# Optimization experiments

Hardware: AMD Instinct MI355X
Metric: run time of the kernel (lower is better)

The kernel has to match this reference:

```python
import jax, jax.numpy as jnp
import numpy as np

DIM = 256
BETA = 4
B, L, L1 = 16, 2048, 4096
EPS = 1e-6


def setup_inputs() -> dict:
    key = jax.random.key(0)
    ks = jax.random.split(key, 20)
    d, db = DIM, DIM // BETA
    s = lambda *sh: 0.02
    inp = {
        "features": jax.random.normal(ks[0], (B, L, d), jnp.float32),
        "quires_box": jax.random.uniform(ks[1], (B, L1, 2), jnp.float32),
        "quires_features": jax.random.normal(ks[2], (B, L1, d), jnp.float32),
        "pos_feature": jax.random.normal(ks[3], (B, L1, d), jnp.float32),
        # contrast1 params
        "c1_w1": jax.random.normal(ks[4], (db, d), jnp.float32) * 0.02,
        "c1_b1": jnp.zeros((db,), jnp.float32),
        "c1_w2": jax.random.normal(ks[5], (d, db), jnp.float32) * 0.02,
        "c1_b2": jnp.zeros((d,), jnp.float32),
        "c1_g": jnp.ones((d,), jnp.float32),
        "c1_be": jnp.zeros((d,), jnp.float32),
        # contrast2 params
        "c2_w1": jax.random.normal(ks[6], (db, d), jnp.float32) * 0.02,
        "c2_b1": jnp.zeros((db,), jnp.float32),
        "c2_w2": jax.random.normal(ks[7], (d, db), jnp.float32) * 0.02,
        "c2_b2": jnp.zeros((d,), jnp.float32),
        "c2_g": jnp.ones((d,), jnp.float32),
        "c2_be": jnp.zeros((d,), jnp.float32),
        # gate MLP (Prediction: Linear(2d->d)+ReLU+Linear(d->2), dropout=identity at eval)
        "g_w1": jax.random.normal(ks[8], (d, 2 * d), jnp.float32) * 0.02,
        "g_b1": jnp.zeros((d,), jnp.float32),
        "g_w2": jax.random.normal(ks[9], (2, d), jnp.float32) * 0.02,
        "g_b2": jnp.zeros((2,), jnp.float32),
    }
    return inp


def _contrast(v1, v2, w1, b1, w2, b2, g, be):
    # v1, v2: [B, N, C]. Pointwise conv1 -> ReLU -> conv2 -> LayerNorm -> sigmoid -> *v1
    v = v1 * v2
    h = jax.nn.relu(jnp.einsum('bnc,dc->bnd', v, w1) + b1)  # [B,N,C/beta]
    u = jnp.einsum('bnd,cd->bnc', h, w2) + b2               # [B,N,C]
    mu = jnp.mean(u, axis=-1, keepdims=True)
    var = jnp.mean(jnp.square(u - mu), axis=-1, keepdims=True)
    ln = (u - mu) * jax.lax.rsqrt(var + EPS) * g + be
    return jax.nn.sigmoid(ln) * v1


def reference(features, quires_box, quires_features, pos_feature,
              c1_w1, c1_b1, c1_w2, c1_b2, c1_g, c1_be,
              c2_w1, c2_b1, c2_w2, c2_b2, c2_g, c2_be,
              g_w1, g_b1, g_w2, g_b2):
    Lf = features.shape[1]
    cx, w = quires_box[..., 0], quires_box[..., 1]
    roi_start = jnp.round(jnp.clip((cx - w / 2) * Lf, 0, Lf - 1)).astype(jnp.int32)
    roi_end = jnp.round(jnp.clip((cx + w / 2) * Lf, 0, Lf - 1)).astype(jnp.int32)
    sf = jnp.take_along_axis(features, roi_start[..., None], axis=1)  # [B,L1,C]
    ef = jnp.take_along_axis(features, roi_end[..., None], axis=1)    # [B,L1,C]
    sf = _contrast(sf, pos_feature, c1_w1, c1_b1, c1_w2, c1_b2, c1_g, c1_be)
    ef = _contrast(ef, pos_feature, c2_w1, c2_b1, c2_w2, c2_b2, c2_g, c2_be)
    pooled = (sf + ef) * 0.5  # aligned_len=True -> mean over the 2 boundaries
    x = jnp.concatenate([pooled, quires_features], axis=-1)  # [B,L1,2C]
    h = jax.nn.relu(jnp.einsum('bnc,dc->bnd', x, g_w1) + g_b1)
    gate = jax.nn.softmax(jnp.einsum('bnd,od->bno', h, g_w2) + g_b2, axis=-1)
    out = pooled * gate[..., 0:1] + quires_features * gate[..., 1:2]
    return jnp.swapaxes(out, 0, 1)  # [L1, B, C]
```

## Files before the change

kernel.cpp:

```cpp
#include <hip/hip_runtime.h>
#include <hip/hip_bf16.h>
#include <math.h>

typedef __attribute__((ext_vector_type(8))) short bf16x8;
typedef __attribute__((ext_vector_type(4))) float f32x4;
typedef __attribute__((ext_vector_type(2))) __fp16 f16x2;
typedef __attribute__((ext_vector_type(4))) unsigned int u32x4;
typedef __attribute__((ext_vector_type(2))) unsigned int u32x2;

constexpr int NB = 16, NQ = 4096, LF = 2048, C = 256;

__device__ __forceinline__ unsigned short bfbits(float x) {
    return __builtin_bit_cast(unsigned short, __float2bfloat16(x));
}
__device__ __forceinline__ unsigned pk2(float a, float b) {
    return (unsigned)bfbits(a) | ((unsigned)bfbits(b) << 16);
}
__device__ __forceinline__ float bflo(unsigned d) { return __builtin_bit_cast(float, d << 16); }
__device__ __forceinline__ float bfhi(unsigned d) { return __builtin_bit_cast(float, d & 0xffff0000u); }
__device__ __forceinline__ unsigned pkh(float a, float b) {
    f16x2 h = __builtin_amdgcn_cvt_pkrtz(a, b);
    return __builtin_bit_cast(unsigned, h);
}
__device__ __forceinline__ float hlo(unsigned u) {
    f16x2 h = __builtin_bit_cast(f16x2, u); return (float)h[0];
}
__device__ __forceinline__ float hhi(unsigned u) {
    f16x2 h = __builtin_bit_cast(f16x2, u); return (float)h[1];
}

__global__ void prep_weights(const float* __restrict__ c1w1, const float* __restrict__ c2w1,
                             const float* __restrict__ c1w2, const float* __restrict__ c2w2,
                             const float* __restrict__ gw1, unsigned short* __restrict__ ws)
{
    int t = blockIdx.x * 256 + threadIdx.x;
    const float* src; int K, nks, dstoff, f;
    if (t < 2048)      { src = c1w1; K = 256; nks = 8;  dstoff = 0;      f = t; }
    else if (t < 4096) { src = c2w1; K = 256; nks = 8;  dstoff = 16384;  f = t - 2048; }
    else if (t < 6144) { src = c1w2; K = 64;  nks = 2;  dstoff = 32768;  f = t - 4096; }
    else if (t < 8192) { src = c2w2; K = 64;  nks = 2;  dstoff = 49152;  f = t - 6144; }
    else               { src = gw1;  K = 512; nks = 16; dstoff = 65536;  f = t - 8192; }
    int l = f & 63, s = f >> 6;
    int nt = s / nks, ks = s % nks;
    int n  = nt * 16 + (l & 15);
    int k0 = ks * 32 + (l >> 4) * 8;
    unsigned short* d = ws + dstoff + (size_t)f * 8;
    const float* sp = src + (size_t)n * K + k0;
    #pragma unroll
    for (int e = 0; e < 8; ++e) d[e] = bfbits(sp[e]);
}

__global__ __launch_bounds__(256, 4)
void semalign_v13(const float* __restrict__ feat,  const float* __restrict__ qbox,
                  const float* __restrict__ qfeat, const float* __restrict__ posf,
                  const float* __restrict__ c1b1,  const float* __restrict__ c1b2,
                  const float* __restrict__ c1g,   const float* __restrict__ c1be,
                  const float* __restrict__ c2b1,  const float* __restrict__ c2b2,
                  const float* __restrict__ c2g,   const float* __restrict__ c2be,
                  const float* __restrict__ gb1,   const float* __restrict__ gw2,
                  const float* __restrict__ gb2,
                  const unsigned short* __restrict__ wsb,
                  float* __restrict__ out)
{
    __shared__ __align__(16) unsigned short sP[4][16][256];

    const int tid = threadIdx.x, l = tid & 63, wid = tid >> 6;
    const int lr = l & 15, lg = l >> 4;
    const int rowb = blockIdx.x * 64 + wid * 16;
    const int q = rowb >> 4;
    const int b = lr;
    const int swz = (lr & 7) << 4;

    const float* prow = posf  + ((size_t)b * NQ + q) * C;
    const float* qrow = qfeat + ((size_t)b * NQ + q) * C;
    float cx = qbox[((size_t)b * NQ + q) * 2 + 0];
    float w  = qbox[((size_t)b * NQ + q) * 2 + 1];
    float fs = fminf(fmaxf((cx - 0.5f * w) * (float)LF, 0.f), (float)(LF - 1));
    float fe = fminf(fmaxf((cx + 0.5f * w) * (float)LF, 0.f), (float)(LF - 1));
    const float* srow = feat + ((size_t)b * LF + (int)rintf(fs)) * C;
    const float* erow = feat + ((size_t)b * LF + (int)rintf(fe)) * C;

    bf16x8 v1f[8], v2f[8];
    #pragma unroll
    for (int ks = 0; ks < 8; ++ks) {
        int k0 = ks * 32 + lg * 8;
        float4 s0 = *(const float4*)(srow + k0), s1 = *(const float4*)(srow + k0 + 4);
        float4 e0 = *(const float4*)(erow + k0), e1 = *(const float4*)(erow + k0 + 4);
        float4 p0 = *(const float4*)(prow + k0), p1 = *(const float4*)(prow + k0 + 4);
        u32x4 a, c;
        a[0] = pk2(s0.x * p0.x, s0.y * p0.y); a[1] = pk2(s0.z * p0.z, s0.w * p0.w);
        a[2] = pk2(s1.x * p1.x, s1.y * p1.y); a[3] = pk2(s1.z * p1.z, s1.w * p1.w);
        c[0] = pk2(e0.x * p0.x, e0.y * p0.y); c[1] = pk2(e0.z * p0.z, e0.w * p0.w);
        c[2] = pk2(e1.x * p1.x, e1.y * p1.y); c[3] = pk2(e1.z * p1.z, e1.w * p1.w);
        v1f[ks] = __builtin_bit_cast(bf16x8, a);
        v2f[ks] = __builtin_bit_cast(bf16x8, c);
    }

    char* pb = (char*)&sP[wid][0][0];
    {
        f32x4 a1[4] = {}, a2[4] = {};
        #pragma unroll
        for (int ks = 0; ks < 8; ++ks) {
            #pragma unroll
            for (int nt = 0; nt < 4; ++nt) {
                bf16x8 wA = *(const bf16x8*)(wsb + ((size_t)((nt * 8 + ks) * 64 + l)) * 8);
                bf16x8 wB = *(const bf16x8*)(wsb + 16384 + ((size_t)((nt * 8 + ks) * 64 + l)) * 8);
                a1[nt] = __builtin_amdgcn_mfma_f32_16x16x32_bf16(wA, v1f[ks], a1[nt], 0, 0, 0);
                a2[nt] = __builtin_amdgcn_mfma_f32_16x16x32_bf16(wB, v2f[ks], a2[nt], 0, 0, 0);
            }
        }
        #pragma unroll
        for (int nt = 0; nt < 4; ++nt) {
            float4 b1v = *(const float4*)(c1b1 + nt * 16 + lg * 4);
            float4 b2v = *(const float4*)(c2b1 + nt * 16 + lg * 4);
            u32x2 wv;
            wv[0] = pk2(fmaxf(a1[nt][0] + b1v.x, 0.f), fmaxf(a1[nt][1] + b1v.y, 0.f));
            wv[1] = pk2(fmaxf(a1[nt][2] + b1v.z, 0.f), fmaxf(a1[nt][3] + b1v.w, 0.f));
            *(u32x2*)(pb + lr * 128 + ((nt * 32 + lg * 8) ^ swz)) = wv;
            wv[0] = pk2(fmaxf(a2[nt][0] + b2v.x, 0.f), fmaxf(a2[nt][1] + b2v.y, 0.f));
            wv[1] = pk2(fmaxf(a2[nt][2] + b2v.z, 0.f), fmaxf(a2[nt][3] + b2v.w, 0.f));
            *(u32x2*)(pb + 2048 + lr * 128 + ((nt * 32 + lg * 8) ^ swz)) = wv;
        }
    }

    f16x2 Ph[16][2];
    #pragma unroll
    for (int j = 0; j < 2; ++j) {
        char* hb = pb + j * 2048;
        asm volatile("s_waitcnt lgkmcnt(0)" ::: "memory");
        bf16x8 hf0 = *(const bf16x8*)(hb + lr * 128 + ((0 + lg * 16) ^ swz));
        bf16x8 hf1 = *(const bf16x8*)(hb + lr * 128 + ((64 + lg * 16) ^ swz));
        const unsigned short* w2b = wsb + (j ? 49152 : 32768);
        const float* b2p = j ? c2b2 : c1b2;
        const float* gp  = j ? c2g  : c1g;
        const float* bep = j ? c2be : c1be;
        const float* xrow = j ? erow : srow;
        float S = 0.f, Q2 = 0.f;

        {
            f32x4 u8[8] = {};
            #pragma unroll
            for (int nt = 0; nt < 8; ++nt) {
                bf16x8 wA = *(const bf16x8*)(w2b + ((size_t)((nt * 2 + 0) * 64 + l)) * 8);
                bf16x8 wB = *(const bf16x8*)(w2b + ((size_t)((nt * 2 + 1) * 64 + l)) * 8);
                u8[nt] = __builtin_amdgcn_mfma_f32_16x16x32_bf16(wA, hf0, u8[nt], 0, 0, 0);
                u8[nt] = __builtin_amdgcn_mfma_f32_16x16x32_bf16(wB, hf1, u8[nt], 0, 0, 0);
            }
            #pragma unroll
            for (int nt = 0; nt < 8; ++nt) {
                float4 bv = *(const float4*)(b2p + nt * 16 + lg * 4);
                u8[nt][0] += bv.x; u8[nt][1] += bv.y; u8[nt][2] += bv.z; u8[nt][3] += bv.w;
                S  += u8[nt][0] + u8[nt][1] + u8[nt][2] + u8[nt][3];
                Q2 += u8[nt][0] * u8[nt][0] + u8[nt][1] * u8[nt][1]
                    + u8[nt][2] * u8[nt][2] + u8[nt][3] * u8[nt][3];
                u32x2 wv;
                wv[0] = pkh(u8[nt][0], u8[nt][1]);
                wv[1] = pkh(u8[nt][2], u8[nt][3]);
                *(u32x2*)(pb + 4096 + nt * 512 + l * 8) = wv;
            }
        }
        f32x4 u8b[8] = {};
        #pragma unroll
        for (int nt = 0; nt < 8; ++nt) {
            bf16x8 wA = *(const bf16x8*)(w2b + ((size_t)(((nt + 8) * 2 + 0) * 64 + l)) * 8);
            bf16x8 wB = *(const bf16x8*)(w2b + ((size_t)(((nt + 8) * 2 + 1) * 64 + l)) * 8);
            u8b[nt] = __builtin_amdgcn_mfma_f32_16x16x32_bf16(wA, hf0, u8b[nt], 0, 0, 0);
            u8b[nt] = __builtin_amdgcn_mfma_f32_16x16x32_bf16(wB, hf1, u8b[nt], 0, 0, 0);
        }
        #pragma unroll
        for (int nt = 0; nt < 8; ++nt) {
            float4 bv = *(const float4*)(b2p + (nt + 8) * 16 + lg * 4);
            u8b[nt][0] += bv.x; u8b[nt][1] += bv.y; u8b[nt][2] += bv.z; u8b[nt][3] += bv.w;
            S  += u8b[nt][0] + u8b[nt][1] + u8b[nt][2] + u8b[nt][3];
            Q2 += u8b[nt][0] * u8b[nt][0] + u8b[nt][1] * u8b[nt][1]
                + u8b[nt][2] * u8b[nt][2] + u8b[nt][3] * u8b[nt][3];
        }
        S  += __shfl_xor(S, 16);  S  += __shfl_xor(S, 32);
        Q2 += __shfl_xor(Q2, 16); Q2 += __shfl_xor(Q2, 32);
        float mu  = S * (1.f / 256.f);
        float rsg = rsqrtf(Q2 * (1.f / 256.f) - mu * mu + 1e-6f);

        u32x2 st[8];
        asm volatile("s_waitcnt lgkmcnt(0)" ::: "memory");
        #pragma unroll
        for (int nt = 0; nt < 8; ++nt)
            st[nt] = *(const u32x2*)(pb + 4096 + nt * 512 + l * 8);
        asm volatile("s_waitcnt lgkmcnt(0)" ::: "memory");

        #pragma unroll
        for (int nt = 0; nt < 16; ++nt) {
            float u4[4];
            if (nt < 8) {
                u4[0] = hlo(st[nt][0]); u4[1] = hhi(st[nt][0]);
                u4[2] = hlo(st[nt][1]); u4[3] = hhi(st[nt][1]);
            } else {
                u4[0] = u8b[nt - 8][0]; u4[1] = u8b[nt - 8][1];
                u4[2] = u8b[nt - 8][2]; u4[3] = u8b[nt - 8][3];
            }
            float4 gv  = *(const float4*)(gp  + nt * 16 + lg * 4);
            float4 bev = *(const float4*)(bep + nt * 16 + lg * 4);
            float4 xv  = *(const float4*)(xrow + nt * 16 + lg * 4);
            float g4[4] = { gv.x, gv.y, gv.z, gv.w };
            float e4[4] = { bev.x, bev.y, bev.z, bev.w };
            float x4[4] = { xv.x, xv.y, xv.z, xv.w };
            float tm[4];
            #pragma unroll
            for (int r = 0; r < 4; ++r) {
                float ln = (u4[r] - mu) * rsg * g4[r] + e4[r];
                float sg = 1.f / (1.f + __expf(-ln));
                tm[r] = 0.5f * sg * x4[r];
            }
            if (j == 0) {
                Ph[nt][0] = __builtin_amdgcn_cvt_pkrtz(tm[0], tm[1]);
                Ph[nt][1] = __builtin_amdgcn_cvt_pkrtz(tm[2], tm[3]);
            } else {
                float p0 = (float)Ph[nt][0][0] + tm[0];
                float p1 = (float)Ph[nt][0][1] + tm[1];
                float p2 = (float)Ph[nt][1][0] + tm[2];
                float p3 = (float)Ph[nt][1][1] + tm[3];
                u32x2 wv;
                wv[0] = pk2(p0, p1); wv[1] = pk2(p2, p3);
                *(u32x2*)(pb + lr * 512 + ((nt * 32 + lg * 8) ^ swz)) = wv;
            }
        }
    }

    bf16x8 xf[16];
    asm volatile("s_waitcnt lgkmcnt(0)" ::: "memory");
    #pragma unroll
    for (int ks = 0; ks < 8; ++ks)
        xf[ks] = *(const bf16x8*)(pb + lr * 512 + ((ks * 64 + lg * 16) ^ swz));
    #pragma unroll
    for (int ks = 0; ks < 8; ++ks) {
        int k0 = ks * 32 + lg * 8;
        float4 q0 = *(const float4*)(qrow + k0), q1 = *(const float4*)(qrow + k0 + 4);
        u32x4 a;
        a[0] = pk2(q0.x, q0.y); a[1] = pk2(q0.z, q0.w);
        a[2] = pk2(q1.x, q1.y); a[3] = pk2(q1.z, q1.w);
        xf[8 + ks] = __builtin_bit_cast(bf16x8, a);
    }

    float t0 = 0.f, t1 = 0.f;
    const unsigned short* gwb = wsb + 65536;
    for (int ntp = 0; ntp < 8; ++ntp) {
        f32x4 ga0 = {}, ga1 = {};
        int n0 = ntp * 2, n1 = ntp * 2 + 1;
        #pragma unroll
        for (int kk = 0; kk < 16; ++kk) {
            bf16x8 wA = *(const bf16x8*)(gwb + ((size_t)((n0 * 16 + kk) * 64 + l)) * 8);
            bf16x8 wB = *(const bf16x8*)(gwb + ((size_t)((n1 * 16 + kk) * 64 + l)) * 8);
            ga0 = __builtin_amdgcn_mfma_f32_16x16x32_bf16(wA, xf[kk], ga0, 0, 0, 0);
            ga1 = __builtin_amdgcn_mfma_f32_16x16x32_bf16(wB, xf[kk], ga1, 0, 0, 0);
        }
        #pragma unroll
        for (int t = 0; t < 2; ++t) {
            f32x4 ga = t ? ga1 : ga0;
            int nt = ntp * 2 + t;
            float4 gbv = *(const float4*)(gb1 + nt * 16 + lg * 4);
            float4 w0v = *(const float4*)(gw2 + nt * 16 + lg * 4);
            float4 w1v = *(const float4*)(gw2 + 256 + nt * 16 + lg * 4);
            float gb4[4] = { gbv.x, gbv.y, gbv.z, gbv.w };
            float w04[4] = { w0v.x, w0v.y, w0v.z, w0v.w };
            float w14[4] = { w1v.x, w1v.y, w1v.z, w1v.w };
            #pragma unroll
            for (int r = 0; r < 4; ++r) {
                float hv = fmaxf(ga[r] + gb4[r], 0.f);
                t0 += hv * w04[r]; t1 += hv * w14[r];
            }
        }
    }
    t0 += __shfl_xor(t0, 16); t0 += __shfl_xor(t0, 32);
    t1 += __shfl_xor(t1, 16); t1 += __shfl_xor(t1, 32);
    float g0 = 1.f / (1.f + __expf((t1 + gb2[1]) - (t0 + gb2[0])));
    float g1 = 1.f - g0;

    float* orow = out + (size_t)(rowb + lr) * C;
    #pragma unroll
    for (int ks = 0; ks < 8; ++ks) {
        u32x4 pu = __builtin_bit_cast(u32x4, xf[ks]);
        u32x4 qu = __builtin_bit_cast(u32x4, xf[8 + ks]);
        float4 o0, o1;
        o0.x = bflo(pu[0]) * g0 + bflo(qu[0]) * g1;
        o0.y = bfhi(pu[0]) * g0 + bfhi(qu[0]) * g1;
        o0.z = bflo(pu[1]) * g0 + bflo(qu[1]) * g1;
        o0.w = bfhi(pu[1]) * g0 + bfhi(qu[1]) * g1;
        o1.x = bflo(pu[2]) * g0 + bflo(qu[2]) * g1;
        o1.y = bfhi(pu[2]) * g0 + bfhi(qu[2]) * g1;
        o1.z = bflo(pu[3]) * g0 + bflo(qu[3]) * g1;
        o1.w = bfhi(pu[3]) * g0 + bfhi(qu[3]) * g1;
        *(float4*)(orow + ks * 32 + lg * 8)     = o0;
        *(float4*)(orow + ks * 32 + lg * 8 + 4) = o1;
    }
}

extern "C" void kernel_launch(void* const* d_in, const int* in_sizes, int n_in,
                              void* d_out, int out_size, void* d_ws, size_t ws_size,
                              hipStream_t stream) {
    const float* feat  = (const float*)d_in[0];
    const float* qbox  = (const float*)d_in[1];
    const float* qfeat = (const float*)d_in[2];
    const float* posf  = (const float*)d_in[3];
    const float* c1w1  = (const float*)d_in[4];
    const float* c1b1  = (const float*)d_in[5];
    const float* c1w2  = (const float*)d_in[6];
    const float* c1b2  = (const float*)d_in[7];
    const float* c1g   = (const float*)d_in[8];
    const float* c1be  = (const float*)d_in[9];
    const float* c2w1  = (const float*)d_in[10];
    const float* c2b1  = (const float*)d_in[11];
    const float* c2w2  = (const float*)d_in[12];
    const float* c2b2  = (const float*)d_in[13];
    const float* c2g   = (const float*)d_in[14];
    const float* c2be  = (const float*)d_in[15];
    const float* gw1   = (const float*)d_in[16];
    const float* gb1   = (const float*)d_in[17];
    const float* gw2   = (const float*)d_in[18];
    const float* gb2   = (const float*)d_in[19];
    float* out = (float*)d_out;
    unsigned short* wsb = (unsigned short*)d_ws;

    prep_weights<<<96, 256, 0, stream>>>(c1w1, c2w1, c1w2, c2w2, gw1, wsb);

    dim3 grid((NB * NQ) / 64), block(256);
    semalign_v13<<<grid, block, 0, stream>>>(
        feat, qbox, qfeat, posf,
        c1b1, c1b2, c1g, c1be,
        c2b1, c2b2, c2g, c2be,
        gb1, gw2, gb2, wsb, out);
}
```

Measured before the change: 176.4 us.

## Restructure gate GEMM to stream K-slices into 16 accumulators, reload inputs for output

The gate MLP GEMM changes loop order. Instead of holding all 16 bf16 input fragments in registers and looping over output tiles, it now streams one K-slice at a time into 16 persistent accumulators. The final blend re-reads the pooled values from LDS and the query features from global memory instead of keeping them in registers. This also uses fp32 query values rather than bf16-rounded ones in the output. The aim is to reshape register pressure and instruction scheduling, at the cost of re-reading the query rows and holding 64 accumulator registers.

```diff
diff --git a/kernel.cpp b/kernel.cpp
--- a/kernel.cpp
+++ b/kernel.cpp
@@ -51,7 +51,7 @@
 }
 
 __global__ __launch_bounds__(256, 4)
-void semalign_v13(const float* __restrict__ feat,  const float* __restrict__ qbox,
+void semalign_v14(const float* __restrict__ feat,  const float* __restrict__ qbox,
                   const float* __restrict__ qfeat, const float* __restrict__ posf,
                   const float* __restrict__ c1b1,  const float* __restrict__ c1b2,
                   const float* __restrict__ c1g,   const float* __restrict__ c1be,
@@ -224,49 +224,43 @@
             }
         }
     }
-
-    bf16x8 xf[16];
     asm volatile("s_waitcnt lgkmcnt(0)" ::: "memory");
-    #pragma unroll
-    for (int ks = 0; ks < 8; ++ks)
-        xf[ks] = *(const bf16x8*)(pb + lr * 512 + ((ks * 64 + lg * 16) ^ swz));
-    #pragma unroll
-    for (int ks = 0; ks < 8; ++ks) {
-        int k0 = ks * 32 + lg * 8;
-        float4 q0 = *(const float4*)(qrow + k0), q1 = *(const float4*)(qrow + k0 + 4);
-        u32x4 a;
-        a[0] = pk2(q0.x, q0.y); a[1] = pk2(q0.z, q0.w);
-        a[2] = pk2(q1.x, q1.y); a[3] = pk2(q1.z, q1.w);
-        xf[8 + ks] = __builtin_bit_cast(bf16x8, a);
+
+    f32x4 ga[16] = {};
+    const unsigned short* gwb = wsb + 65536;
+    #pragma clang loop unroll(disable)
+    for (int kk = 0; kk < 16; ++kk) {
+        bf16x8 xk;
+        if (kk < 8) {
+            xk = *(const bf16x8*)(pb + lr * 512 + ((kk * 64 + lg * 16) ^ swz));
+        } else {
+            int k0 = (kk - 8) * 32 + lg * 8;
+            float4 q0 = *(const float4*)(qrow + k0), q1 = *(const float4*)(qrow + k0 + 4);
+            u32x4 a;
+            a[0] = pk2(q0.x, q0.y); a[1] = pk2(q0.z, q0.w);
+            a[2] = pk2(q1.x, q1.y); a[3] = pk2(q1.z, q1.w);
+            xk = __builtin_bit_cast(bf16x8, a);
+        }
+        #pragma unroll
+        for (int nt = 0; nt < 16; ++nt) {
+            bf16x8 wf = *(const bf16x8*)(gwb + ((size_t)((nt * 16 + kk) * 64 + l)) * 8);
+            ga[nt] = __builtin_amdgcn_mfma_f32_16x16x32_bf16(wf, xk, ga[nt], 0, 0, 0);
+        }
     }
 
     float t0 = 0.f, t1 = 0.f;
-    const unsigned short* gwb = wsb + 65536;
-    for (int ntp = 0; ntp < 8; ++ntp) {
-        f32x4 ga0 = {}, ga1 = {};
-        int n0 = ntp * 2, n1 = ntp * 2 + 1;
-        #pragma unroll
-        for (int kk = 0; kk < 16; ++kk) {
-            bf16x8 wA = *(const bf16x8*)(gwb + ((size_t)((n0 * 16 + kk) * 64 + l)) * 8);
-            bf16x8 wB = *(const bf16x8*)(gwb + ((size_t)((n1 * 16 + kk) * 64 + l)) * 8);
-            ga0 = __builtin_amdgcn_mfma_f32_16x16x32_bf16(wA, xf[kk], ga0, 0, 0, 0);
-            ga1 = __builtin_amdgcn_mfma_f32_16x16x32_bf16(wB, xf[kk], ga1, 0, 0, 0);
-        }
-        #pragma unroll
-        for (int t = 0; t < 2; ++t) {
-            f32x4 ga = t ? ga1 : ga0;
-            int nt = ntp * 2 + t;
-            float4 gbv = *(const float4*)(gb1 + nt * 16 + lg * 4);
-            float4 w0v = *(const float4*)(gw2 + nt * 16 + lg * 4);
-            float4 w1v = *(const float4*)(gw2 + 256 + nt * 16 + lg * 4);
-            float gb4[4] = { gbv.x, gbv.y, gbv.z, gbv.w };
-            float w04[4] = { w0v.x, w0v.y, w0v.z, w0v.w };
-            float w14[4] = { w1v.x, w1v.y, w1v.z, w1v.w };
-            #pragma unroll
-            for (int r = 0; r < 4; ++r) {
-                float hv = fmaxf(ga[r] + gb4[r], 0.f);
-                t0 += hv * w04[r]; t1 += hv * w14[r];
-            }
+    #pragma unroll
+    for (int nt = 0; nt < 16; ++nt) {
+        float4 gbv = *(const float4*)(gb1 + nt * 16 + lg * 4);
+        float4 w0v = *(const float4*)(gw2 + nt * 16 + lg * 4);
+        float4 w1v = *(const float4*)(gw2 + 256 + nt * 16 + lg * 4);
+        float gb4[4] = { gbv.x, gbv.y, gbv.z, gbv.w };
+        float w04[4] = { w0v.x, w0v.y, w0v.z, w0v.w };
+        float w14[4] = { w1v.x, w1v.y, w1v.z, w1v.w };
+        #pragma unroll
+        for (int r = 0; r < 4; ++r) {
+            float hv = fmaxf(ga[nt][r] + gb4[r], 0.f);
+            t0 += hv * w04[r]; t1 += hv * w14[r];
         }
     }
     t0 += __shfl_xor(t0, 16); t0 += __shfl_xor(t0, 32);
@@ -277,17 +271,19 @@
     float* orow = out + (size_t)(rowb + lr) * C;
     #pragma unroll
     for (int ks = 0; ks < 8; ++ks) {
-        u32x4 pu = __builtin_bit_cast(u32x4, xf[ks]);
-        u32x4 qu = __builtin_bit_cast(u32x4, xf[8 + ks]);
+        bf16x8 pf = *(const bf16x8*)(pb + lr * 512 + ((ks * 64 + lg * 16) ^ swz));
+        u32x4 pu = __builtin_bit_cast(u32x4, pf);
+        int k0 = ks * 32 + lg * 8;
+        float4 q0 = *(const float4*)(qrow + k0), q1 = *(const float4*)(qrow + k0 + 4);
         float4 o0, o1;
-        o0.x = bflo(pu[0]) * g0 + bflo(qu[0]) * g1;
-        o0.y = bfhi(pu[0]) * g0 + bfhi(qu[0]) * g1;
-        o0.z = bflo(pu[1]) * g0 + bflo(qu[1]) * g1;
-        o0.w = bfhi(pu[1]) * g0 + bfhi(qu[1]) * g1;
-        o1.x = bflo(pu[2]) * g0 + bflo(qu[2]) * g1;
-        o1.y = bfhi(pu[2]) * g0 + bfhi(qu[2]) * g1;
-        o1.z = bflo(pu[3]) * g0 + bflo(qu[3]) * g1;
-        o1.w = bfhi(pu[3]) * g0 + bfhi(qu[3]) * g1;
+        o0.x = bflo(pu[0]) * g0 + q0.x * g1;
+        o0.y = bfhi(pu[0]) * g0 + q0.y * g1;
+        o0.z = bflo(pu[1]) * g0 + q0.z * g1;
+        o0.w = bfhi(pu[1]) * g0 + q0.w * g1;
+        o1.x = bflo(pu[2]) * g0 + q1.x * g1;
+        o1.y = bfhi(pu[2]) * g0 + q1.y * g1;
+        o1.z = bflo(pu[3]) * g0 + q1.z * g1;
+        o1.w = bfhi(pu[3]) * g0 + q1.w * g1;
         *(float4*)(orow + ks * 32 + lg * 8)     = o0;
         *(float4*)(orow + ks * 32 + lg * 8 + 4) = o1;
     }
@@ -322,7 +318,7 @@
     prep_weights<<<96, 256, 0, stream>>>(c1w1, c2w1, c1w2, c2w2, gw1, wsb);
 
     dim3 grid((NB * NQ) / 64), block(256);
-    semalign_v13<<<grid, block, 0, stream>>>(
+    semalign_v14<<<grid, block, 0, stream>>>(
         feat, qbox, qfeat, posf,
         c1b1, c1b2, c1g, c1be,
         c2b1, c2b2, c2g, c2be,
```

Measured after the change: 164.1 us. 7.0% less time.
